# Optimization experiments

Measured on AMD Instinct MI355X. Metric: run time of the kernel, lower is better.

## Reference

```python
import jax, jax.numpy as jnp
import numpy as np

N_NODES = 50000
N_EDGES = 500000
IN_CH = 128
HID = 64
HEADS = 4
N_LAYERS = 3
OUT_CH = 16
N_GRAPHS = 64
NEG_SLOPE = 0.2  # PyG GATConv default


def setup_inputs() -> dict:
    key = jax.random.key(0)
    ks = jax.random.split(key, 20)
    inp = {
        'x': jax.random.normal(ks[0], (N_NODES, IN_CH), dtype=jnp.float32),
        'edge_attr': jax.random.normal(ks[1], (N_EDGES, 8), dtype=jnp.float32),
        'edge_index': jax.random.randint(ks[2], (2, N_EDGES), 0, N_NODES, dtype=jnp.int64),
        'batch': jnp.sort(jax.random.randint(ks[3], (N_NODES,), 0, N_GRAPHS, dtype=jnp.int64)),
    }
    kidx = 4
    in_dim = IN_CH
    for i in range(N_LAYERS):
        inp[f'W{i}'] = jax.random.normal(ks[kidx], (in_dim, HEADS * HID), dtype=jnp.float32) * (1.0 / np.sqrt(in_dim)); kidx += 1
        inp[f'asrc{i}'] = jax.random.normal(ks[kidx], (HEADS, HID), dtype=jnp.float32) * 0.1; kidx += 1
        inp[f'adst{i}'] = jax.random.normal(ks[kidx], (HEADS, HID), dtype=jnp.float32) * 0.1; kidx += 1
        inp[f'b{i}'] = jnp.zeros((HEADS * HID,), dtype=jnp.float32)
        in_dim = HEADS * HID
    inp['Wc'] = jax.random.normal(ks[kidx], (HEADS * HID, OUT_CH), dtype=jnp.float32) * (1.0 / np.sqrt(HEADS * HID)); kidx += 1
    inp['bc'] = jnp.zeros((OUT_CH,), dtype=jnp.float32)
    return inp


def _gat_layer(x, src, dst, W, asrc, adst, b):
    # x: [N, F_in] -> h: [N, H, C]
    N = x.shape[0]
    h = (x @ W).reshape(N, HEADS, HID)
    s_src = jnp.einsum('nhc,hc->nh', h, asrc)  # [N, H]
    s_dst = jnp.einsum('nhc,hc->nh', h, adst)
    e = jax.nn.leaky_relu(s_src[src] + s_dst[dst], NEG_SLOPE)  # [E, H]
    # segment softmax over incoming edges of each destination node
    m = jax.ops.segment_max(e, dst, num_segments=N)            # [N, H]
    ex = jnp.exp(e - m[dst])
    denom = jax.ops.segment_sum(ex, dst, num_segments=N)       # [N, H]
    alpha = ex / (denom[dst] + 1e-16)                           # [E, H]
    out = jax.ops.segment_sum(alpha[:, :, None] * h[src], dst, num_segments=N)  # [N, H, C]
    return out.reshape(N, HEADS * HID) + b


def reference(x, edge_attr, edge_index, batch,
              W0, asrc0, adst0, b0,
              W1, asrc1, adst1, b1,
              W2, asrc2, adst2, b2,
              Wc, bc):
    N = x.shape[0]
    loop = jnp.arange(N, dtype=edge_index.dtype)
    # PyG GATConv adds self-loops by default
    src = jnp.concatenate([edge_index[0], loop])
    dst = jnp.concatenate([edge_index[1], loop])
    params = [(W0, asrc0, adst0, b0), (W1, asrc1, adst1, b1), (W2, asrc2, adst2, b2)]
    h = x
    for (W, asrc, adst, b) in params:
        h = jax.nn.relu(_gat_layer(h, src, dst, W, asrc, adst, b))
        # nn.Dropout(0.5) is identity in eval mode
    pooled = jax.ops.segment_sum(h, batch, num_segments=N_GRAPHS)  # global_add_pool
    return pooled @ Wc + bc
```

## Files before the change

### kernel.cpp

```cpp
#include <hip/hip_runtime.h>
#include <hip/hip_bf16.h>

#define NNODES 50000
#define NEDGES 500000
#define INCH 128
#define HID 64
#define HEADS 4
#define FDIM 256
#define NGRAPHS 64
#define OUTCH 16
#define NEG_SLOPE 0.2f

#define BM 128
#define BN 256
#define BK 32

typedef float f32x4 __attribute__((ext_vector_type(4)));
typedef _Float16 f16x8 __attribute__((ext_vector_type(8)));
typedef _Float16 f16x4 __attribute__((ext_vector_type(4)));

__device__ inline void gld_lds16(const void* g, void* l) {
    __builtin_amdgcn_global_load_lds((__attribute__((address_space(1))) void*)g,
                                     (__attribute__((address_space(3))) void*)l, 16, 0, 0);
}


__global__ void k_hist(const int* __restrict__ dst, int E, int* __restrict__ counts) {
    int i = blockIdx.x * blockDim.x + threadIdx.x;
    if (i < E) atomicAdd(&counts[dst[i]], 1);
}

__global__ __launch_bounds__(256) void k_blocksum(const int* __restrict__ counts, int N,
                                                  int* __restrict__ bsum) {
    int idx = blockIdx.x * 256 + threadIdx.x;
    int v = (idx < N) ? counts[idx] : 0;
#pragma unroll
    for (int off = 32; off; off >>= 1) v += __shfl_xor(v, off);
    __shared__ int wsum[4];
    if ((threadIdx.x & 63) == 0) wsum[threadIdx.x >> 6] = v;
    __syncthreads();
    if (threadIdx.x == 0) bsum[blockIdx.x] = wsum[0] + wsum[1] + wsum[2] + wsum[3];
}

__global__ __launch_bounds__(256) void k_scanfinal(const int* __restrict__ counts,
                                                   const int* __restrict__ bsum, int N,
                                                   int* __restrict__ rowstart,
                                                   int* __restrict__ cursor) {
    __shared__ int tmp[256];
    __shared__ int wsum[4];
    int t = threadIdx.x, b = blockIdx.x;
    int p = 0;
    for (int i = t; i < b; i += 256) p += bsum[i];
#pragma unroll
    for (int off = 32; off; off >>= 1) p += __shfl_xor(p, off);
    int idx = b * 256 + t;
    int v = (idx < N) ? counts[idx] : 0;
    tmp[t] = v;
    if ((t & 63) == 0) wsum[t >> 6] = p;
    __syncthreads();
    int bp = wsum[0] + wsum[1] + wsum[2] + wsum[3];
    for (int off = 1; off < 256; off <<= 1) {
        int u = (t >= off) ? tmp[t - off] : 0;
        __syncthreads();
        tmp[t] += u;
        __syncthreads();
    }
    if (idx < N) {
        int incl = bp + tmp[t];
        rowstart[idx + 1] = incl;
        cursor[idx] = incl - v;
    }
    if (idx == 0) rowstart[0] = 0;
}

__global__ void k_scatter(const int* __restrict__ src, const int* __restrict__ dst, int E,
                          int* __restrict__ cursor, int* __restrict__ csr_src) {
    int i = blockIdx.x * blockDim.x + threadIdx.x;
    if (i < E) {
        int p = atomicAdd(&cursor[dst[i]], 1);
        csr_src[p] = src[i];
    }
}


__global__ void k_wdecomp(const float* __restrict__ W, _Float16* __restrict__ Wt, int K) {
    int i = blockIdx.x * 256 + threadIdx.x;
    if (i >= K * 256) return;
    int k = i >> 8, n = i & 255;
    Wt[n * K + k] = (_Float16)W[i];
}


__global__ void k_adecomp(const float* __restrict__ X, _Float16* __restrict__ Xf, int total4) {
    int i = blockIdx.x * 256 + threadIdx.x;
    if (i >= total4) return;
    float4 v = ((const float4*)X)[i];
    f16x4 o = {(_Float16)v.x, (_Float16)v.y, (_Float16)v.z, (_Float16)v.w};
    ((f16x4*)Xf)[i] = o;
}


__global__ __launch_bounds__(256, 2) void k_gemm_mfma(
    const _Float16* __restrict__ A, const _Float16* __restrict__ B,
    const float* __restrict__ av, const float* __restrict__ dv,
    _Float16* __restrict__ Hf,
    float* __restrict__ ssrcO, float* __restrict__ sdstO, int M, int K) {
    __shared__ _Float16 sA[2][BM * BK];
    __shared__ _Float16 sB[2][BN * BK];

    const int t = threadIdx.x;
    const int row0 = blockIdx.x * BM;
    const int wv = t >> 6, ln = t & 63, lr = ln & 15, lk = ln >> 4;

    const int ar = wv * 16 + (ln >> 2);
    const int alc = (ln & 3) ^ ((ar >> 1) & 3);
    const size_t agoff0 = (size_t)min(row0 + ar, M - 1) * K + alc * 8;
    const size_t agoff1 = (size_t)min(row0 + ar + 64, M - 1) * K + alc * 8;
    const int fsc = lk ^ ((lr >> 1) & 3);

    f32x4 acc[8][4] = {};
    const int nt = K / BK;

#define STAGE(tt, p)                                                        \
    do {                                                                    \
        int _k0 = (tt)*BK;                                                  \
        gld_lds16(A + agoff0 + _k0, &sA[p][wv * 512]);                      \
        gld_lds16(A + agoff1 + _k0, &sA[p][2048 + wv * 512]);               \
        _Pragma("unroll") for (int _j = 0; _j < 4; ++_j) {                  \
            int _br = _j * 64 + ar;                                         \
            gld_lds16(B + (size_t)_br * K + _k0 + alc * 8,                  \
                      &sB[p][_j * 2048 + wv * 512]);                        \
        }                                                                   \
    } while (0)

    STAGE(0, 0);
    __syncthreads();
    for (int tt = 0; tt < nt; ++tt) {
        int cur = tt & 1;
        if (tt + 1 < nt) STAGE(tt + 1, cur ^ 1);

        f16x8 af[8];
#pragma unroll
        for (int mi = 0; mi < 8; ++mi)
            af[mi] = *(const f16x8*)&sA[cur][(mi * 16 + lr) * BK + fsc * 8];
#pragma unroll
        for (int ni = 0; ni < 4; ++ni) {
            f16x8 bf = *(const f16x8*)&sB[cur][(wv * 64 + ni * 16 + lr) * BK + fsc * 8];
#pragma unroll
            for (int mi = 0; mi < 8; ++mi)
                acc[mi][ni] = __builtin_amdgcn_mfma_f32_16x16x32_f16(af[mi], bf, acc[mi][ni], 0, 0, 0);
        }
        __syncthreads();
    }
#undef STAGE

    float avr[4], dvr[4];
#pragma unroll
    for (int ni = 0; ni < 4; ++ni) {
        int col = wv * 64 + ni * 16 + lr;
        avr[ni] = av[col];
        dvr[ni] = dv[col];
    }
#pragma unroll
    for (int mi = 0; mi < 8; ++mi) {
        float ps[4] = {}, pd[4] = {};
        int rbase = row0 + mi * 16 + lk * 4;
#pragma unroll
        for (int ni = 0; ni < 4; ++ni) {
            int col = wv * 64 + ni * 16 + lr;
            f32x4 v = acc[mi][ni];
#pragma unroll
            for (int j = 0; j < 4; ++j) {
                if (rbase + j < M) Hf[(size_t)(rbase + j) * FDIM + col] = (_Float16)v[j];
                ps[j] += v[j] * avr[ni];
                pd[j] += v[j] * dvr[ni];
            }
        }
#pragma unroll
        for (int j = 0; j < 4; ++j) {
            float s = ps[j], q = pd[j];
            s += __shfl_xor(s, 1); s += __shfl_xor(s, 2);
            s += __shfl_xor(s, 4); s += __shfl_xor(s, 8);
            q += __shfl_xor(q, 1); q += __shfl_xor(q, 2);
            q += __shfl_xor(q, 4); q += __shfl_xor(q, 8);
            if (lr == 0 && rbase + j < M) {
                ssrcO[(rbase + j) * HEADS + wv] = s;
                sdstO[(rbase + j) * HEADS + wv] = q;
            }
        }
    }
}


__global__ __launch_bounds__(256) void k_edgew(
    const float* __restrict__ ssrc, const float* __restrict__ sdst,
    const int* __restrict__ rowstart, const int* __restrict__ csr_src,
    float* __restrict__ wcsr, float* __restrict__ aself, int N) {
    int tid = blockIdx.x * 256 + threadIdx.x;
    int n = tid >> 2, h = tid & 3;
    if (n >= N) return;
    int r0 = rowstart[n], r1 = rowstart[n + 1];
    float sd = sdst[n * HEADS + h];
    float es = ssrc[n * HEADS + h] + sd;
    es = (es > 0.f) ? es : NEG_SLOPE * es;
    float m = es;
    for (int r = r0; r < r1; ++r) {
        int s = csr_src[r];
        float sc = ssrc[s * HEADS + h] + sd;
        sc = (sc > 0.f) ? sc : NEG_SLOPE * sc;
        m = fmaxf(m, sc);
    }
    float denom = __expf(es - m);
    for (int r = r0; r < r1; ++r) {
        int s = csr_src[r];
        float sc = ssrc[s * HEADS + h] + sd;
        sc = (sc > 0.f) ? sc : NEG_SLOPE * sc;
        float w = __expf(sc - m);
        wcsr[r * HEADS + h] = w;
        denom += w;
    }
    float inv = 1.0f / denom;
    aself[n * HEADS + h] = __expf(es - m) * inv;
    for (int r = r0; r < r1; ++r) wcsr[r * HEADS + h] *= inv;
}


__global__ __launch_bounds__(256) void k_aggregate(
    const _Float16* __restrict__ hf,
    const float* __restrict__ wcsr, const float* __restrict__ aself,
    const int* __restrict__ rowstart, const int* __restrict__ csr_src,
    const float* __restrict__ bias,
    _Float16* __restrict__ outf, int N) {
    int wv = threadIdx.x >> 6, ln = threadIdx.x & 63;
    int n = blockIdx.x * 4 + wv;
    if (n >= N) return;
    int head = ln >> 4;
    int fo = head * 64 + (ln & 15) * 4;
    float a0 = aself[n * HEADS + head];
    f16x4 sv = *(const f16x4*)&hf[(size_t)n * FDIM + fo];
    float4 acc = make_float4(a0 * (float)sv[0], a0 * (float)sv[1],
                             a0 * (float)sv[2], a0 * (float)sv[3]);
    int r0 = rowstart[n], r1 = rowstart[n + 1];
    int cnt = r1 - r0;
    for (int base = 0; base < cnt; base += 8) {
        int s[8];
        float w[8];
        f16x4 u[8];
#pragma unroll
        for (int i = 0; i < 8; ++i) {
            int rr = min(r0 + base + i, r1 - 1);
            s[i] = csr_src[rr];
            w[i] = wcsr[rr * HEADS + head];
        }
#pragma unroll
        for (int i = 0; i < 8; ++i) u[i] = *(const f16x4*)&hf[(size_t)s[i] * FDIM + fo];
#pragma unroll
        for (int i = 0; i < 8; ++i) w[i] = (base + i < cnt) ? w[i] : 0.f;
#pragma unroll
        for (int i = 0; i < 8; ++i) {
            acc.x += w[i] * (float)u[i][0];
            acc.y += w[i] * (float)u[i][1];
            acc.z += w[i] * (float)u[i][2];
            acc.w += w[i] * (float)u[i][3];
        }
    }
    float4 bv = *(const float4*)&bias[fo];
    f16x4 o;
    o[0] = (_Float16)fmaxf(acc.x + bv.x, 0.f);
    o[1] = (_Float16)fmaxf(acc.y + bv.y, 0.f);
    o[2] = (_Float16)fmaxf(acc.z + bv.z, 0.f);
    o[3] = (_Float16)fmaxf(acc.w + bv.w, 0.f);
    *(f16x4*)&outf[(size_t)n * FDIM + fo] = o;
}


__global__ __launch_bounds__(256) void k_pool(const _Float16* __restrict__ hf,
                                              const int* __restrict__ batch,
                                              float* __restrict__ pooled, int N) {
    int f = threadIdx.x;
    int n0 = blockIdx.x * 128;
    if (n0 >= N) return;
    int n1 = min(n0 + 128, N);
    int g = batch[n0];
    float run = 0.f;
    for (int n = n0; n < n1; ++n) {
        int gn = batch[n];
        if (gn != g) {
            atomicAdd(&pooled[g * FDIM + f], run);
            run = 0.f;
            g = gn;
        }
        run += (float)hf[(size_t)n * FDIM + f];
    }
    atomicAdd(&pooled[g * FDIM + f], run);
}


__global__ __launch_bounds__(256) void k_final(const float* __restrict__ pooled,
                                               const float* __restrict__ Wc,
                                               const float* __restrict__ bc,
                                               float* __restrict__ out) {
    int tid = blockIdx.x * 256 + threadIdx.x;
    int g = tid >> 4, o = tid & 15;
    float s = bc[o];
    for (int k = 0; k < FDIM; ++k) s += pooled[g * FDIM + k] * Wc[k * OUTCH + o];
    out[g * OUTCH + o] = s;
}


extern "C" void kernel_launch(void* const* d_in, const int* in_sizes, int n_in,
                              void* d_out, int out_size, void* d_ws, size_t ws_size,
                              hipStream_t stream) {
    const float* x = (const float*)d_in[0];
    const int* edge_index = (const int*)d_in[2];
    const int* batch = (const int*)d_in[3];
    const float* W[3]    = {(const float*)d_in[4], (const float*)d_in[8],  (const float*)d_in[12]};
    const float* asrc[3] = {(const float*)d_in[5], (const float*)d_in[9],  (const float*)d_in[13]};
    const float* adst[3] = {(const float*)d_in[6], (const float*)d_in[10], (const float*)d_in[14]};
    const float* bias[3] = {(const float*)d_in[7], (const float*)d_in[11], (const float*)d_in[15]};
    const float* Wc = (const float*)d_in[16];
    const float* bc = (const float*)d_in[17];

    const int N = in_sizes[3];
    const int E = in_sizes[2] / 2;
    const int* e_src = edge_index;
    const int* e_dst = edge_index + E;

    char* ws = (char*)d_ws;
    size_t off = 0;
    _Float16* hb = (_Float16*)(ws + off); off += (size_t)N * FDIM * 2;
    _Float16* xf = (_Float16*)(ws + off); off += (size_t)N * INCH * 2;
    _Float16* P  = (_Float16*)(ws + off); off += (size_t)N * FDIM * 2;
    float* ssrc = (float*)(ws + off); off += (size_t)N * HEADS * 4;
    float* sdst = (float*)(ws + off); off += (size_t)N * HEADS * 4;
    float* wcsr = (float*)(ws + off); off += (size_t)E * HEADS * 4;
    float* aself = (float*)(ws + off); off += (size_t)N * HEADS * 4;
    int* rowstart = (int*)(ws + off); off += ((size_t)(N + 1) * 4 + 255) / 256 * 256;
    int* counts = (int*)(ws + off); off += (size_t)N * 4;
    int* cursor = (int*)(ws + off); off += (size_t)N * 4;
    int* csr_src = (int*)(ws + off); off += (size_t)E * 4;
    float* pooled = (float*)(ws + off); off += (size_t)NGRAPHS * FDIM * 4;
    int* bsum = (int*)(ws + off); off += ((size_t)((N + 255) / 256) * 4 + 255) / 256 * 256;
    _Float16* Wt[3];
    int Ks[3] = {INCH, FDIM, FDIM};
    for (int l = 0; l < 3; ++l) {
        Wt[l] = (_Float16*)(ws + off); off += (size_t)256 * Ks[l] * 2;
    }

    const int nb = (N + 255) / 256;

    hipMemsetAsync(counts, 0, (size_t)N * 4, stream);
    k_hist<<<(E + 255) / 256, 256, 0, stream>>>(e_dst, E, counts);
    k_blocksum<<<nb, 256, 0, stream>>>(counts, N, bsum);
    k_scanfinal<<<nb, 256, 0, stream>>>(counts, bsum, N, rowstart, cursor);
    k_scatter<<<(E + 255) / 256, 256, 0, stream>>>(e_src, e_dst, E, cursor, csr_src);

    k_adecomp<<<((N * INCH / 4) + 255) / 256, 256, 0, stream>>>(x, xf, N * INCH / 4);
    for (int l = 0; l < 3; ++l)
        k_wdecomp<<<(Ks[l] * 256 + 255) / 256, 256, 0, stream>>>(W[l], Wt[l], Ks[l]);

    const _Float16* Af = xf;
    for (int l = 0; l < 3; ++l) {
        int K = Ks[l];
        k_gemm_mfma<<<(N + BM - 1) / BM, 256, 0, stream>>>(Af, Wt[l], asrc[l], adst[l],
                                                           hb, ssrc, sdst, N, K);
        k_edgew<<<(N * HEADS + 255) / 256, 256, 0, stream>>>(ssrc, sdst, rowstart, csr_src,
                                                             wcsr, aself, N);
        k_aggregate<<<(N + 3) / 4, 256, 0, stream>>>(hb, wcsr, aself, rowstart, csr_src,
                                                     bias[l], P, N);
        Af = P;
    }

    hipMemsetAsync(pooled, 0, (size_t)NGRAPHS * FDIM * 4, stream);
    k_pool<<<(N + 127) / 128, 256, 0, stream>>>(P, batch, pooled, N);
    k_final<<<4, 256, 0, stream>>>(pooled, Wc, bc, (float*)d_out);
}
```

Baseline: 386.4 us.

## Halve GEMM tile rows, stage output through LDS, vectorize edge softmax per node

The GEMM tile shrinks from 128 to 64 rows, which doubles the block count and halves the accumulators. The epilogue now writes the fp16 tile into swizzled LDS and stores full 16-byte rows to global memory, then computes the attention scores from LDS instead of using shuffle reductions. k_edgew now handles all four heads per thread with float4 loads and drops the third pass that normalized the weights. Normalization is deferred to k_aggregate, which multiplies by a stored inverse denominator. The trade-off is fewer threads in the edge kernel, one fewer global rewrite of the edge weights, and more LDS traffic in the GEMM epilogue.

```diff
diff --git a/kernel.cpp b/kernel.cpp
--- a/kernel.cpp
+++ b/kernel.cpp
@@ -11,7 +11,7 @@
 #define OUTCH 16
 #define NEG_SLOPE 0.2f
 
-#define BM 128
+#define BM 64
 #define BN 256
 #define BK 32
 
@@ -100,7 +100,7 @@
 }
 
 
-__global__ __launch_bounds__(256, 2) void k_gemm_mfma(
+__global__ __launch_bounds__(256) void k_gemm_mfma(
     const _Float16* __restrict__ A, const _Float16* __restrict__ B,
     const float* __restrict__ av, const float* __restrict__ dv,
     _Float16* __restrict__ Hf,
@@ -114,18 +114,16 @@
 
     const int ar = wv * 16 + (ln >> 2);
     const int alc = (ln & 3) ^ ((ar >> 1) & 3);
-    const size_t agoff0 = (size_t)min(row0 + ar, M - 1) * K + alc * 8;
-    const size_t agoff1 = (size_t)min(row0 + ar + 64, M - 1) * K + alc * 8;
+    const size_t agoff = (size_t)min(row0 + ar, M - 1) * K + alc * 8;
     const int fsc = lk ^ ((lr >> 1) & 3);
 
-    f32x4 acc[8][4] = {};
+    f32x4 acc[4][4] = {};
     const int nt = K / BK;
 
 #define STAGE(tt, p)                                                        \
     do {                                                                    \
         int _k0 = (tt)*BK;                                                  \
-        gld_lds16(A + agoff0 + _k0, &sA[p][wv * 512]);                      \
-        gld_lds16(A + agoff1 + _k0, &sA[p][2048 + wv * 512]);               \
+        gld_lds16(A + agoff + _k0, &sA[p][wv * 512]);                       \
         _Pragma("unroll") for (int _j = 0; _j < 4; ++_j) {                  \
             int _br = _j * 64 + ar;                                         \
             gld_lds16(B + (size_t)_br * K + _k0 + alc * 8,                  \
@@ -139,54 +137,62 @@
         int cur = tt & 1;
         if (tt + 1 < nt) STAGE(tt + 1, cur ^ 1);
 
-        f16x8 af[8];
-#pragma unroll
-        for (int mi = 0; mi < 8; ++mi)
+        f16x8 af[4];
+#pragma unroll
+        for (int mi = 0; mi < 4; ++mi)
             af[mi] = *(const f16x8*)&sA[cur][(mi * 16 + lr) * BK + fsc * 8];
 #pragma unroll
         for (int ni = 0; ni < 4; ++ni) {
             f16x8 bf = *(const f16x8*)&sB[cur][(wv * 64 + ni * 16 + lr) * BK + fsc * 8];
 #pragma unroll
-            for (int mi = 0; mi < 8; ++mi)
+            for (int mi = 0; mi < 4; ++mi)
                 acc[mi][ni] = __builtin_amdgcn_mfma_f32_16x16x32_f16(af[mi], bf, acc[mi][ni], 0, 0, 0);
         }
         __syncthreads();
     }
 #undef STAGE
 
-    float avr[4], dvr[4];
-#pragma unroll
-    for (int ni = 0; ni < 4; ++ni) {
-        int col = wv * 64 + ni * 16 + lr;
-        avr[ni] = av[col];
-        dvr[ni] = dv[col];
-    }
-#pragma unroll
-    for (int mi = 0; mi < 8; ++mi) {
-        float ps[4] = {}, pd[4] = {};
-        int rbase = row0 + mi * 16 + lk * 4;
+    _Float16* Hs = (_Float16*)sB;
+#pragma unroll
+    for (int mi = 0; mi < 4; ++mi) {
 #pragma unroll
         for (int ni = 0; ni < 4; ++ni) {
             int col = wv * 64 + ni * 16 + lr;
-            f32x4 v = acc[mi][ni];
+            int cc = col >> 3;
 #pragma unroll
             for (int j = 0; j < 4; ++j) {
-                if (rbase + j < M) Hf[(size_t)(rbase + j) * FDIM + col] = (_Float16)v[j];
-                ps[j] += v[j] * avr[ni];
-                pd[j] += v[j] * dvr[ni];
+                int row = mi * 16 + lk * 4 + j;
+                Hs[row * 256 + ((cc ^ (row & 7)) << 3) + (col & 7)] = (_Float16)acc[mi][ni][j];
             }
         }
-#pragma unroll
-        for (int j = 0; j < 4; ++j) {
-            float s = ps[j], q = pd[j];
-            s += __shfl_xor(s, 1); s += __shfl_xor(s, 2);
-            s += __shfl_xor(s, 4); s += __shfl_xor(s, 8);
-            q += __shfl_xor(q, 1); q += __shfl_xor(q, 2);
-            q += __shfl_xor(q, 4); q += __shfl_xor(q, 8);
-            if (lr == 0 && rbase + j < M) {
-                ssrcO[(rbase + j) * HEADS + wv] = s;
-                sdstO[(rbase + j) * HEADS + wv] = q;
+    }
+    __syncthreads();
+
+#pragma unroll
+    for (int i = 0; i < 8; ++i) {
+        int f = i * 256 + t;
+        int row = f >> 5, ccl = f & 31;
+        if (row0 + row < M)
+            *(f16x8*)(Hf + (size_t)(row0 + row) * FDIM + ccl * 8) =
+                *(const f16x8*)&Hs[row * 256 + ((ccl ^ (row & 7)) << 3)];
+    }
+
+    {
+        int srow = t >> 2, head = t & 3;
+        if (row0 + srow < M) {
+            float s = 0.f, q = 0.f;
+#pragma unroll
+            for (int j = 0; j < 8; ++j) {
+                f16x8 hv = *(const f16x8*)&Hs[srow * 256 + (((head * 8 + j) ^ (srow & 7)) << 3)];
+#pragma unroll
+                for (int e = 0; e < 8; ++e) {
+                    float x = (float)hv[e];
+                    s += x * av[head * 64 + j * 8 + e];
+                    q += x * dv[head * 64 + j * 8 + e];
+                }
             }
+            ssrcO[(row0 + srow) * HEADS + head] = s;
+            sdstO[(row0 + srow) * HEADS + head] = q;
         }
     }
 }
@@ -195,39 +201,57 @@
 __global__ __launch_bounds__(256) void k_edgew(
     const float* __restrict__ ssrc, const float* __restrict__ sdst,
     const int* __restrict__ rowstart, const int* __restrict__ csr_src,
-    float* __restrict__ wcsr, float* __restrict__ aself, int N) {
-    int tid = blockIdx.x * 256 + threadIdx.x;
-    int n = tid >> 2, h = tid & 3;
+    float* __restrict__ wcsr, float* __restrict__ selfw, float* __restrict__ winv, int N) {
+    int n = blockIdx.x * 256 + threadIdx.x;
     if (n >= N) return;
     int r0 = rowstart[n], r1 = rowstart[n + 1];
-    float sd = sdst[n * HEADS + h];
-    float es = ssrc[n * HEADS + h] + sd;
-    es = (es > 0.f) ? es : NEG_SLOPE * es;
-    float m = es;
+    float4 sd = *(const float4*)&sdst[n * 4];
+    float4 es = *(const float4*)&ssrc[n * 4];
+    es.x += sd.x; es.y += sd.y; es.z += sd.z; es.w += sd.w;
+    es.x = (es.x > 0.f) ? es.x : NEG_SLOPE * es.x;
+    es.y = (es.y > 0.f) ? es.y : NEG_SLOPE * es.y;
+    es.z = (es.z > 0.f) ? es.z : NEG_SLOPE * es.z;
+    es.w = (es.w > 0.f) ? es.w : NEG_SLOPE * es.w;
+    float4 m = es;
     for (int r = r0; r < r1; ++r) {
         int s = csr_src[r];
-        float sc = ssrc[s * HEADS + h] + sd;
-        sc = (sc > 0.f) ? sc : NEG_SLOPE * sc;
-        m = fmaxf(m, sc);
-    }
-    float denom = __expf(es - m);
+        float4 sc = *(const float4*)&ssrc[s * 4];
+        sc.x += sd.x; sc.y += sd.y; sc.z += sd.z; sc.w += sd.w;
+        sc.x = (sc.x > 0.f) ? sc.x : NEG_SLOPE * sc.x;
+        sc.y = (sc.y > 0.f) ? sc.y : NEG_SLOPE * sc.y;
+        sc.z = (sc.z > 0.f) ? sc.z : NEG_SLOPE * sc.z;
+        sc.w = (sc.w > 0.f) ? sc.w : NEG_SLOPE * sc.w;
+        m.x = fmaxf(m.x, sc.x); m.y = fmaxf(m.y, sc.y);
+        m.z = fmaxf(m.z, sc.z); m.w = fmaxf(m.w, sc.w);
+    }
+    float4 ws;
+    ws.x = __expf(es.x - m.x); ws.y = __expf(es.y - m.y);
+    ws.z = __expf(es.z - m.z); ws.w = __expf(es.w - m.w);
+    float4 den = ws;
     for (int r = r0; r < r1; ++r) {
         int s = csr_src[r];
-        float sc = ssrc[s * HEADS + h] + sd;
-        sc = (sc > 0.f) ? sc : NEG_SLOPE * sc;
-        float w = __expf(sc - m);
-        wcsr[r * HEADS + h] = w;
-        denom += w;
-    }
-    float inv = 1.0f / denom;
-    aself[n * HEADS + h] = __expf(es - m) * inv;
-    for (int r = r0; r < r1; ++r) wcsr[r * HEADS + h] *= inv;
+        float4 sc = *(const float4*)&ssrc[s * 4];
+        sc.x += sd.x; sc.y += sd.y; sc.z += sd.z; sc.w += sd.w;
+        sc.x = (sc.x > 0.f) ? sc.x : NEG_SLOPE * sc.x;
+        sc.y = (sc.y > 0.f) ? sc.y : NEG_SLOPE * sc.y;
+        sc.z = (sc.z > 0.f) ? sc.z : NEG_SLOPE * sc.z;
+        sc.w = (sc.w > 0.f) ? sc.w : NEG_SLOPE * sc.w;
+        float4 w;
+        w.x = __expf(sc.x - m.x); w.y = __expf(sc.y - m.y);
+        w.z = __expf(sc.z - m.z); w.w = __expf(sc.w - m.w);
+        *(float4*)&wcsr[r * 4] = w;
+        den.x += w.x; den.y += w.y; den.z += w.z; den.w += w.w;
+    }
+    *(float4*)&selfw[n * 4] = ws;
+    float4 iv = make_float4(1.f / den.x, 1.f / den.y, 1.f / den.z, 1.f / den.w);
+    *(float4*)&winv[n * 4] = iv;
 }
 
 
 __global__ __launch_bounds__(256) void k_aggregate(
     const _Float16* __restrict__ hf,
-    const float* __restrict__ wcsr, const float* __restrict__ aself,
+    const float* __restrict__ wcsr, const float* __restrict__ selfw,
+    const float* __restrict__ winv,
     const int* __restrict__ rowstart, const int* __restrict__ csr_src,
     const float* __restrict__ bias,
     _Float16* __restrict__ outf, int N) {
@@ -236,7 +260,8 @@
     if (n >= N) return;
     int head = ln >> 4;
     int fo = head * 64 + (ln & 15) * 4;
-    float a0 = aself[n * HEADS + head];
+    float a0 = selfw[n * 4 + head];
+    float inv = winv[n * 4 + head];
     f16x4 sv = *(const f16x4*)&hf[(size_t)n * FDIM + fo];
     float4 acc = make_float4(a0 * (float)sv[0], a0 * (float)sv[1],
                              a0 * (float)sv[2], a0 * (float)sv[3]);
@@ -250,7 +275,7 @@
         for (int i = 0; i < 8; ++i) {
             int rr = min(r0 + base + i, r1 - 1);
             s[i] = csr_src[rr];
-            w[i] = wcsr[rr * HEADS + head];
+            w[i] = wcsr[rr * 4 + head];
         }
 #pragma unroll
         for (int i = 0; i < 8; ++i) u[i] = *(const f16x4*)&hf[(size_t)s[i] * FDIM + fo];
@@ -266,10 +291,10 @@
     }
     float4 bv = *(const float4*)&bias[fo];
     f16x4 o;
-    o[0] = (_Float16)fmaxf(acc.x + bv.x, 0.f);
-    o[1] = (_Float16)fmaxf(acc.y + bv.y, 0.f);
-    o[2] = (_Float16)fmaxf(acc.z + bv.z, 0.f);
-    o[3] = (_Float16)fmaxf(acc.w + bv.w, 0.f);
+    o[0] = (_Float16)fmaxf(acc.x * inv + bv.x, 0.f);
+    o[1] = (_Float16)fmaxf(acc.y * inv + bv.y, 0.f);
+    o[2] = (_Float16)fmaxf(acc.z * inv + bv.z, 0.f);
+    o[3] = (_Float16)fmaxf(acc.w * inv + bv.w, 0.f);
     *(f16x4*)&outf[(size_t)n * FDIM + fo] = o;
 }
 
@@ -334,7 +359,8 @@
     float* ssrc = (float*)(ws + off); off += (size_t)N * HEADS * 4;
     float* sdst = (float*)(ws + off); off += (size_t)N * HEADS * 4;
     float* wcsr = (float*)(ws + off); off += (size_t)E * HEADS * 4;
-    float* aself = (float*)(ws + off); off += (size_t)N * HEADS * 4;
+    float* selfw = (float*)(ws + off); off += (size_t)N * HEADS * 4;
+    float* winv = (float*)(ws + off); off += (size_t)N * HEADS * 4;
     int* rowstart = (int*)(ws + off); off += ((size_t)(N + 1) * 4 + 255) / 256 * 256;
     int* counts = (int*)(ws + off); off += (size_t)N * 4;
     int* cursor = (int*)(ws + off); off += (size_t)N * 4;
@@ -364,10 +390,10 @@
         int K = Ks[l];
         k_gemm_mfma<<<(N + BM - 1) / BM, 256, 0, stream>>>(Af, Wt[l], asrc[l], adst[l],
                                                            hb, ssrc, sdst, N, K);
-        k_edgew<<<(N * HEADS + 255) / 256, 256, 0, stream>>>(ssrc, sdst, rowstart, csr_src,
-                                                             wcsr, aself, N);
-        k_aggregate<<<(N + 3) / 4, 256, 0, stream>>>(hb, wcsr, aself, rowstart, csr_src,
-                                                     bias[l], P, N);
+        k_edgew<<<(N + 255) / 256, 256, 0, stream>>>(ssrc, sdst, rowstart, csr_src,
+                                                     wcsr, selfw, winv, N);
+        k_aggregate<<<(N + 3) / 4, 256, 0, stream>>>(hb, wcsr, selfw, winv, rowstart,
+                                                     csr_src, bias[l], P, N);
         Af = P;
     }
 
```

Result: slower. 411.5 us (+6.5%).
